# Optimization experiments

Hardware: AMD Instinct MI355X
Metric: run time of the kernel (lower is better)

Reference implementation:

```python
import math
import jax, jax.numpy as jnp
import numpy as np

N_NODES = 100000
N_EDGES = 1600000
IN_DIM, HID_DIM, OUT_DIM = 8, 64, 112


def _glorot(key, fan_in, fan_out):
    lim = math.sqrt(6.0 / (fan_in + fan_out))
    return jax.random.uniform(key, (fan_in, fan_out), jnp.float32, -lim, lim)


def _layer_params(key, in_d, out_d):
    ks = jax.random.split(key, 8)
    return dict(
        Wq=_glorot(ks[0], in_d, out_d), bq=jnp.zeros((out_d,), jnp.float32),
        Wk=_glorot(ks[1], in_d, out_d), bk=jnp.zeros((out_d,), jnp.float32),
        Wv=_glorot(ks[2], in_d, out_d), bv=jnp.zeros((out_d,), jnp.float32),
        Ws=_glorot(ks[3], in_d, out_d), bs=jnp.zeros((out_d,), jnp.float32),
    )


def setup_inputs() -> dict:
    key = jax.random.key(0)
    kx, ke, k0, k1, k2 = jax.random.split(key, 5)
    inp = {
        'x': jax.random.normal(kx, (N_NODES, IN_DIM), jnp.float32),
        'edge_index': jax.random.randint(ke, (2, N_EDGES), 0, N_NODES, jnp.int64),
    }
    for li, (kk, ind, outd) in enumerate([(k0, IN_DIM, HID_DIM), (k1, HID_DIM, HID_DIM), (k2, HID_DIM, OUT_DIM)]):
        p = _layer_params(kk, ind, outd)
        for name, v in p.items():
            inp[f'{name}{li}'] = v
    return inp


def _transformer_conv(x, src, dst, Wq, bq, Wk, bk, Wv, bv, Ws, bs):
    # heads=1, concat=True, no edge_attr, eval mode (no dropout)
    N = x.shape[0]
    C = Wq.shape[1]
    q = x @ Wq + bq            # [N, C]
    k = x @ Wk + bk
    v = x @ Wv + bv
    # per-edge attention score: <q_dst, k_src> / sqrt(C)
    scores = jnp.sum(q[dst] * k[src], axis=-1) * (1.0 / math.sqrt(C))  # [E]
    # segment softmax over destination neighborhoods (stable)
    m = jax.ops.segment_max(scores, dst, num_segments=N)               # [N]
    e = jnp.exp(scores - m[dst])                                       # [E]
    denom = jax.ops.segment_sum(e, dst, num_segments=N)                # [N]
    alpha = e / denom[dst]                                             # [E]
    # weighted scatter-add of source values to destinations
    out = jax.ops.segment_sum(alpha[:, None] * v[src], dst, num_segments=N)  # [N, C]
    # root/skip connection
    return out + (x @ Ws + bs)


def reference(x, edge_index,
              Wq0, bq0, Wk0, bk0, Wv0, bv0, Ws0, bs0,
              Wq1, bq1, Wk1, bk1, Wv1, bv1, Ws1, bs1,
              Wq2, bq2, Wk2, bk2, Wv2, bv2, Ws2, bs2):
    src, dst = edge_index[0], edge_index[1]
    h = _transformer_conv(x, src, dst, Wq0, bq0, Wk0, bk0, Wv0, bv0, Ws0, bs0)
    h = jax.nn.relu(h)
    h = _transformer_conv(h, src, dst, Wq1, bq1, Wk1, bk1, Wv1, bv1, Ws1, bs1)
    h = jax.nn.relu(h)
    out = _transformer_conv(h, src, dst, Wq2, bq2, Wk2, bk2, Wv2, bv2, Ws2, bs2)
    return out
```

## Files before the change

kernel.cpp:

```cpp
#include <hip/hip_runtime.h>
#include <hip/hip_fp16.h>
#include <math.h>
#include <float.h>
#include <stdint.h>

#define NN 100000
#define NE 1600000

#define SCAN_T 256
#define SCAN_E 1024
#define SCAN_NB ((NN + SCAN_E - 1) / SCAN_E)

#define NBUCK ((NN + 255) / 256)
#define EPB   4096
#define NBLK  ((NE + EPB - 1) / EPB)
#define HISTN (NBUCK * NBLK)
#define GS_NB ((HISTN + SCAN_E - 1) / SCAN_E)
#define BCAP  5120

typedef __attribute__((ext_vector_type(8))) short short8v;
typedef __attribute__((ext_vector_type(4))) float float4v;

__device__ __forceinline__ unsigned short f32_to_bf16_rne(float f) {
    unsigned u = __float_as_uint(f);
    u += 0x7FFFu + ((u >> 16) & 1u);
    return (unsigned short)(u >> 16);
}
__device__ __forceinline__ float bf16_to_f32(unsigned short h) {
    return __uint_as_float(((unsigned)h) << 16);
}

__device__ __forceinline__ void prep_one(int idx, int K, int OUT,
    const float* Wq, const float* Wk, const float* Wv, const float* Ws,
    unsigned short* wsp) {
    int NKS  = (K + 31) / 32;
    int j    = idx & 7;
    int lane = (idx >> 3) & 63;
    int cell = idx >> 9;
    int ks   = cell % NKS;
    int ct   = cell / NKS;
    int g = lane >> 4, ln = lane & 15;
    int k = ks * 32 + g * 8 + j;
    int c = ct * 16 + ln;
    int mat = c / OUT, cm = c % OUT;
    const float* W = (mat == 0) ? Wq : (mat == 1) ? Wk : (mat == 2) ? Wv : Ws;
    float f = (k < K) ? W[(size_t)k * OUT + cm] : 0.f;
    unsigned short h = f32_to_bf16_rne(f);
    float resid = f - bf16_to_f32(h);
    wsp[(size_t)cell * 1024 + lane * 8 + j]       = h;
    wsp[(size_t)cell * 1024 + 512 + lane * 8 + j] = f32_to_bf16_rne(resid);
}

#define PREP_N0 (16 * 1 * 512)
#define PREP_N1 (16 * 2 * 512)
#define PREP_N2 (28 * 2 * 512)
#define PREP_NT (PREP_N0 + PREP_N1 + PREP_N2)

__global__ __launch_bounds__(256)
void prep_w_all(const float* __restrict__ q0W, const float* __restrict__ k0W,
                const float* __restrict__ v0W, const float* __restrict__ s0W,
                const float* __restrict__ q1W, const float* __restrict__ k1W,
                const float* __restrict__ v1W, const float* __restrict__ s1W,
                const float* __restrict__ q2W, const float* __restrict__ k2W,
                const float* __restrict__ v2W, const float* __restrict__ s2W,
                unsigned short* __restrict__ wsp0,
                unsigned short* __restrict__ wsp1,
                unsigned short* __restrict__ wsp2) {
    int idx = blockIdx.x * 256 + threadIdx.x;
    if (idx < PREP_N0)
        prep_one(idx, 8, 64, q0W, k0W, v0W, s0W, wsp0);
    else if (idx < PREP_N0 + PREP_N1)
        prep_one(idx - PREP_N0, 64, 64, q1W, k1W, v1W, s1W, wsp1);
    else if (idx < PREP_NT)
        prep_one(idx - PREP_N0 - PREP_N1, 64, 112, q2W, k2W, v2W, s2W, wsp2);
}

template<int K, int OUT, int CTSPLIT>
__global__ __launch_bounds__(256)
void gemm_qkvs(const float* __restrict__ x,
               const unsigned short* __restrict__ wsp,
               const float* __restrict__ bq, const float* __restrict__ bk,
               const float* __restrict__ bv, const float* __restrict__ bs,
               float* __restrict__ q, unsigned short* __restrict__ kv,
               float* __restrict__ outskip) {
    constexpr int NKS  = (K + 31) / 32;
    constexpr int OUTT = 4 * OUT;
    constexpr int NCT  = OUTT / 16;
    constexpr int CTPB = NCT / CTSPLIT;

    const int t    = threadIdx.x;
    const int lane = t & 63;
    const int wv   = t >> 6;
    const int g    = lane >> 4;
    const int ln   = lane & 15;
    const int rowbase = (blockIdx.x * 4 + wv) * 32;
    if (rowbase >= NN) return;

    union F8 { short8v v; unsigned short s[8]; uint4 u4; };

    F8 ahi[2][NKS], alo[2][NKS];
#pragma unroll
    for (int rt = 0; rt < 2; ++rt) {
        int r = rowbase + rt * 16 + ln;
        if (r >= NN) r = NN - 1;
        const float* rowp = x + (size_t)r * K;
#pragma unroll
        for (int ks = 0; ks < NKS; ++ks) {
            const int k0 = ks * 32 + g * 8;
            float xv[8];
            if (k0 + 8 <= K) {
                float4 p0 = *(const float4*)(rowp + k0);
                float4 p1 = *(const float4*)(rowp + k0 + 4);
                xv[0] = p0.x; xv[1] = p0.y; xv[2] = p0.z; xv[3] = p0.w;
                xv[4] = p1.x; xv[5] = p1.y; xv[6] = p1.z; xv[7] = p1.w;
            } else {
#pragma unroll
                for (int j = 0; j < 8; ++j) xv[j] = 0.f;
            }
#pragma unroll
            for (int j = 0; j < 8; ++j) {
                unsigned short h = f32_to_bf16_rne(xv[j]);
                ahi[rt][ks].s[j] = h;
                alo[rt][ks].s[j] = f32_to_bf16_rne(xv[j] - bf16_to_f32(h));
            }
        }
    }

    const int ct0 = blockIdx.y * CTPB;
#pragma unroll 1
    for (int ct = ct0; ct < ct0 + CTPB; ++ct) {
        F8 bhi[NKS], blo[NKS];
        const unsigned short* wp = wsp + (size_t)(ct * NKS) * 1024 + lane * 8;
#pragma unroll
        for (int ks = 0; ks < NKS; ++ks) {
            bhi[ks].u4 = *(const uint4*)(wp + ks * 1024);
            blo[ks].u4 = *(const uint4*)(wp + ks * 1024 + 512);
        }

        const int cb  = ct * 16;
        const int mat = cb / OUT;
        const int cm  = (cb % OUT) + ln;
        const float* B = (mat == 0) ? bq : (mat == 1) ? bk : (mat == 2) ? bv : bs;
        const float bias = B[cm];
        float4v acc0 = {bias, bias, bias, bias};
        float4v acc1 = {bias, bias, bias, bias};
#pragma unroll
        for (int ks = 0; ks < NKS; ++ks) {
            acc0 = __builtin_amdgcn_mfma_f32_16x16x32_bf16(ahi[0][ks].v, blo[ks].v, acc0, 0, 0, 0);
            acc0 = __builtin_amdgcn_mfma_f32_16x16x32_bf16(alo[0][ks].v, bhi[ks].v, acc0, 0, 0, 0);
            acc0 = __builtin_amdgcn_mfma_f32_16x16x32_bf16(ahi[0][ks].v, bhi[ks].v, acc0, 0, 0, 0);
            acc1 = __builtin_amdgcn_mfma_f32_16x16x32_bf16(ahi[1][ks].v, blo[ks].v, acc1, 0, 0, 0);
            acc1 = __builtin_amdgcn_mfma_f32_16x16x32_bf16(alo[1][ks].v, bhi[ks].v, acc1, 0, 0, 0);
            acc1 = __builtin_amdgcn_mfma_f32_16x16x32_bf16(ahi[1][ks].v, bhi[ks].v, acc1, 0, 0, 0);
        }

        if (mat == 0 || mat == 3) {
            float* dst = (mat == 0) ? q : outskip;
#pragma unroll
            for (int rt = 0; rt < 2; ++rt) {
                float4v a = rt ? acc1 : acc0;
#pragma unroll
                for (int reg = 0; reg < 4; ++reg) {
                    int node = rowbase + rt * 16 + g * 4 + reg;
                    if (node < NN)
                        dst[(size_t)node * OUT + cm] = a[reg];
                }
            }
        } else {
            const int base = (mat == 1) ? 0 : 4;
            const int kvoff = ((cm >> 2) * 8) + (cm & 3) + base;
#pragma unroll
            for (int rt = 0; rt < 2; ++rt) {
                float4v a = rt ? acc1 : acc0;
#pragma unroll
                for (int reg = 0; reg < 4; ++reg) {
                    int node = rowbase + rt * 16 + g * 4 + reg;
                    float f = a[reg];
                    float other = __shfl_xor(f, 1);
                    if (node < NN && !(ln & 1)) {
                        unsigned lo16 = __half_as_ushort(__float2half_rn(f));
                        unsigned hi16 = __half_as_ushort(__float2half_rn(other));
                        *(unsigned*)(kv + (size_t)node * (2 * OUT) + kvoff)
                            = lo16 | (hi16 << 16);
                    }
                }
            }
        }
    }
}

__global__ __launch_bounds__(256)
void bin_count(const int* __restrict__ ei, int* __restrict__ hist) {
    __shared__ int h[NBUCK];
    const int t = threadIdx.x;
    for (int i = t; i < NBUCK; i += 256) h[i] = 0;
    __syncthreads();
    int e0 = blockIdx.x * EPB;
    int e1 = e0 + EPB < NE ? e0 + EPB : NE;
    for (int i = e0 + t; i < e1; i += 256)
        atomicAdd(&h[ei[NE + i] >> 8], 1);
    __syncthreads();
    for (int i = t; i < NBUCK; i += 256)
        hist[(size_t)i * NBLK + blockIdx.x] = h[i];
}

__global__ __launch_bounds__(SCAN_T)
void gscan1(int* __restrict__ a, int* __restrict__ bsums) {
    __shared__ int lds[SCAN_T];
    int t = threadIdx.x;
    int base = blockIdx.x * SCAN_E + t * 4;
    int vals[4];
    int s = 0;
#pragma unroll
    for (int j = 0; j < 4; ++j) {
        int idx = base + j;
        vals[j] = (idx < HISTN) ? a[idx] : 0;
        s += vals[j];
    }
    lds[t] = s;
    __syncthreads();
    for (int off = 1; off < SCAN_T; off <<= 1) {
        int xx = (t >= off) ? lds[t - off] : 0;
        __syncthreads();
        lds[t] += xx;
        __syncthreads();
    }
    int run = (t > 0) ? lds[t - 1] : 0;
    if (t == SCAN_T - 1) bsums[blockIdx.x] = lds[t];
#pragma unroll
    for (int j = 0; j < 4; ++j) {
        int idx = base + j;
        if (idx < HISTN) a[idx] = run;
        run += vals[j];
    }
}

__global__ __launch_bounds__(256)
void gscan2(int* __restrict__ bsums) {
    __shared__ int lds[256];
    int t = threadIdx.x;
    lds[t] = (t < GS_NB) ? bsums[t] : 0;
    __syncthreads();
    for (int off = 1; off < 256; off <<= 1) {
        int xx = (t >= off) ? lds[t - off] : 0;
        __syncthreads();
        lds[t] += xx;
        __syncthreads();
    }
    if (t < GS_NB) bsums[t] = (t > 0) ? lds[t - 1] : 0;
}

__global__ __launch_bounds__(256)
void gscan3(int* __restrict__ a, const int* __restrict__ bsums,
            int* __restrict__ bstart) {
    int i = blockIdx.x * 256 + threadIdx.x;
    if (i < HISTN) {
        int v = a[i] + bsums[i / SCAN_E];
        a[i] = v;
        if (i % NBLK == 0) bstart[i / NBLK] = v;
    }
    if (i == 0) bstart[NBUCK] = NE;
}

__global__ __launch_bounds__(256)
void bin_scatter(const int* __restrict__ ei, const int* __restrict__ hist,
                 unsigned* __restrict__ ebuf) {
    __shared__ int off[NBUCK];
    const int t = threadIdx.x;
    for (int i = t; i < NBUCK; i += 256)
        off[i] = hist[(size_t)i * NBLK + blockIdx.x];
    __syncthreads();
    int e0 = blockIdx.x * EPB;
    int e1 = e0 + EPB < NE ? e0 + EPB : NE;
    for (int i = e0 + t; i < e1; i += 256) {
        int src = ei[i];
        int dst = ei[NE + i];
        int b = dst >> 8;
        int p = atomicAdd(&off[b], 1);
        ebuf[p] = ((unsigned)(dst & 255) << 17) | (unsigned)src;
    }
}

__global__ __launch_bounds__(256)
void bucket_hist(const int* __restrict__ bstart,
                 const unsigned* __restrict__ ebuf,
                 int* __restrict__ counts) {
    __shared__ int h[256];
    const int b = blockIdx.x;
    const int t = threadIdx.x;
    h[t] = 0;
    __syncthreads();
    int beg = bstart[b], end = bstart[b + 1];
    for (int i = beg + t; i < end; i += 256)
        atomicAdd(&h[ebuf[i] >> 17], 1);
    __syncthreads();
    int d = b * 256 + t;
    if (d < NN) counts[d] = h[t];
}

__global__ __launch_bounds__(SCAN_T)
void scan1(const int* __restrict__ counts, int* __restrict__ offsets,
           int* __restrict__ blocksums) {
    __shared__ int lds[SCAN_T];
    int t = threadIdx.x;
    int base = blockIdx.x * SCAN_E + t * 4;
    int vals[4];
    int s = 0;
#pragma unroll
    for (int j = 0; j < 4; ++j) {
        int idx = base + j;
        vals[j] = (idx < NN) ? counts[idx] : 0;
        s += vals[j];
    }
    lds[t] = s;
    __syncthreads();
    for (int off = 1; off < SCAN_T; off <<= 1) {
        int xx = (t >= off) ? lds[t - off] : 0;
        __syncthreads();
        lds[t] += xx;
        __syncthreads();
    }
    int run = (t > 0) ? lds[t - 1] : 0;
    if (t == SCAN_T - 1) blocksums[blockIdx.x] = lds[t];
#pragma unroll
    for (int j = 0; j < 4; ++j) {
        int idx = base + j;
        if (idx < NN) offsets[idx] = run;
        run += vals[j];
    }
}

__global__ __launch_bounds__(128)
void scan2(int* __restrict__ blocksums) {
    __shared__ int lds[128];
    int t = threadIdx.x;
    lds[t] = (t < SCAN_NB) ? blocksums[t] : 0;
    __syncthreads();
    for (int off = 1; off < 128; off <<= 1) {
        int xx = (t >= off) ? lds[t - off] : 0;
        __syncthreads();
        lds[t] += xx;
        __syncthreads();
    }
    if (t < SCAN_NB) blocksums[t] = (t > 0) ? lds[t - 1] : 0;
}

__global__ __launch_bounds__(256)
void scan3(int* __restrict__ offsets, const int* __restrict__ blocksums) {
    int i = blockIdx.x * blockDim.x + threadIdx.x;
    if (i < NN) offsets[i] = offsets[i] + blocksums[i / SCAN_E];
    if (i == 0) offsets[NN] = NE;
}

__global__ __launch_bounds__(256)
void csr_write(const int* __restrict__ bstart,
               const unsigned* __restrict__ ebuf,
               const int* __restrict__ offsets,
               int* __restrict__ sorted_src) {
    __shared__ int h[256];
    __shared__ int pre[256];
    __shared__ int posi[256];
    __shared__ unsigned srt[BCAP];
    const int b = blockIdx.x;
    const int t = threadIdx.x;
    h[t] = 0;
    __syncthreads();
    int beg = bstart[b];
    int cnt = bstart[b + 1] - beg;
    cnt = cnt < BCAP ? cnt : BCAP;
    const unsigned* buf = ebuf + beg;
    for (int i = t; i < cnt; i += 256)
        atomicAdd(&h[buf[i] >> 17], 1);
    __syncthreads();
    int v = h[t];
    pre[t] = v;
    __syncthreads();
    for (int off = 1; off < 256; off <<= 1) {
        int xx = (t >= off) ? pre[t - off] : 0;
        __syncthreads();
        pre[t] += xx;
        __syncthreads();
    }
    posi[t] = pre[t] - v;
    __syncthreads();
    for (int i = t; i < cnt; i += 256) {
        unsigned u = buf[i];
        int dl = u >> 17;
        int p = atomicAdd(&posi[dl], 1);
        srt[p] = u & 0x1FFFFu;
    }
    __syncthreads();
    const int base = offsets[b << 8];
    for (int i = t; i < cnt; i += 256)
        sorted_src[base + i] = (int)srt[i];
}

__device__ __forceinline__ float row16_sum(float x) {
    int y;
    y = __builtin_amdgcn_update_dpp(0, __float_as_int(x), 0x121, 0xF, 0xF, true); x += __int_as_float(y);
    y = __builtin_amdgcn_update_dpp(0, __float_as_int(x), 0x122, 0xF, 0xF, true); x += __int_as_float(y);
    y = __builtin_amdgcn_update_dpp(0, __float_as_int(x), 0x124, 0xF, 0xF, true); x += __int_as_float(y);
    y = __builtin_amdgcn_update_dpp(0, __float_as_int(x), 0x128, 0xF, 0xF, true); x += __int_as_float(y);
    return x;
}

__device__ __forceinline__ float mix2(float acc, unsigned u, float q0, float q1) {
    __half2 h = *(__half2*)&u;
    acc = fmaf(__half2float(h.x), q0, acc);
    return fmaf(__half2float(h.y), q1, acc);
}
__device__ __forceinline__ void vmix2(float& a0, float& a1, unsigned u, float w) {
    __half2 h = *(__half2*)&u;
    a0 = fmaf(__half2float(h.x), w, a0);
    a1 = fmaf(__half2float(h.y), w, a1);
}

template<int C, bool RELU>
__global__ __launch_bounds__(128)
void attn_gather(const int* __restrict__ offsets,
                 const int* __restrict__ sorted_src,
                 const float* __restrict__ q,
                 const unsigned short* __restrict__ kv,
                 float* __restrict__ out, float scale) {
    const int wid  = (int)((blockIdx.x * blockDim.x + threadIdx.x) >> 6);
    const int lane = threadIdx.x & 63;
    if (wid >= NN) return;
    const int grp = lane >> 4;
    const int ch  = (lane & 15) * 4;
    constexpr bool P2 = (C > 64);
    const bool hi = P2 && (ch + 64 < C);

    const int beg = offsets[wid], end = offsets[wid + 1];

    const float sl = scale * 1.44269504f;
    float4 qv0 = *(const float4*)(q + (size_t)wid * C + ch);
    qv0.x *= sl; qv0.y *= sl; qv0.z *= sl; qv0.w *= sl;
    float4 qv1 = make_float4(0.f, 0.f, 0.f, 0.f);
    if (hi) {
        qv1 = *(const float4*)(q + (size_t)wid * C + ch + 64);
        qv1.x *= sl; qv1.y *= sl; qv1.z *= sl; qv1.w *= sl;
    }

    float m = -FLT_MAX, l = 0.f;
    float4 a0 = make_float4(0.f, 0.f, 0.f, 0.f);
    float4 a1 = make_float4(0.f, 0.f, 0.f, 0.f);

    const unsigned short* kvch = kv + 2 * ch;
    const uint4 zz = make_uint4(0, 0, 0, 0);

    int i = beg + grp;
    while (i < end) {
        uint4 t0[4], t1[4];
#pragma unroll
        for (int j = 0; j < 4; ++j) {
            t0[j] = zz; t1[j] = zz;
            int idx = i + 4 * j;
            if (idx < end) {
                const unsigned short* row = kvch + (size_t)sorted_src[idx] * (2 * C);
                t0[j] = *(const uint4*)(row);
                if (hi) t1[j] = *(const uint4*)(row + 128);
            }
        }
        float s[4];
#pragma unroll
        for (int j = 0; j < 4; ++j) {
            float part = 0.f;
            part = mix2(part, t0[j].x, qv0.x, qv0.y);
            part = mix2(part, t0[j].y, qv0.z, qv0.w);
            if (P2) {
                part = mix2(part, t1[j].x, qv1.x, qv1.y);
                part = mix2(part, t1[j].y, qv1.z, qv1.w);
            }
            part = row16_sum(part);
            s[j] = (i + 4 * j < end) ? part : -FLT_MAX;
        }
        float mn = fmaxf(m, fmaxf(fmaxf(s[0], s[1]), fmaxf(s[2], s[3])));
        float al = __builtin_amdgcn_exp2f(m - mn);
        float w[4];
#pragma unroll
        for (int j = 0; j < 4; ++j)
            w[j] = __builtin_amdgcn_exp2f(s[j] - mn);
        l = l * al + ((w[0] + w[1]) + (w[2] + w[3]));
        a0.x *= al; a0.y *= al; a0.z *= al; a0.w *= al;
        if (P2) { a1.x *= al; a1.y *= al; a1.z *= al; a1.w *= al; }
#pragma unroll
        for (int j = 0; j < 4; ++j) {
            vmix2(a0.x, a0.y, t0[j].z, w[j]);
            vmix2(a0.z, a0.w, t0[j].w, w[j]);
            if (P2) {
                vmix2(a1.x, a1.y, t1[j].z, w[j]);
                vmix2(a1.z, a1.w, t1[j].w, w[j]);
            }
        }
        m = mn;
        i += 16;
    }

#pragma unroll
    for (int d = 16; d <= 32; d <<= 1) {
        float mo = __shfl_xor(m, d);
        float lo = __shfl_xor(l, d);
        float4 ao0, ao1;
        ao0.x = __shfl_xor(a0.x, d); ao0.y = __shfl_xor(a0.y, d);
        ao0.z = __shfl_xor(a0.z, d); ao0.w = __shfl_xor(a0.w, d);
        if (P2) {
            ao1.x = __shfl_xor(a1.x, d); ao1.y = __shfl_xor(a1.y, d);
            ao1.z = __shfl_xor(a1.z, d); ao1.w = __shfl_xor(a1.w, d);
        }
        float mn = fmaxf(m, mo);
        float e1 = (l  > 0.f) ? __builtin_amdgcn_exp2f(m  - mn) : 0.f;
        float e2 = (lo > 0.f) ? __builtin_amdgcn_exp2f(mo - mn) : 0.f;
        l = l * e1 + lo * e2;
        a0.x = a0.x * e1 + ao0.x * e2; a0.y = a0.y * e1 + ao0.y * e2;
        a0.z = a0.z * e1 + ao0.z * e2; a0.w = a0.w * e1 + ao0.w * e2;
        if (P2) {
            a1.x = a1.x * e1 + ao1.x * e2; a1.y = a1.y * e1 + ao1.y * e2;
            a1.z = a1.z * e1 + ao1.z * e2; a1.w = a1.w * e1 + ao1.w * e2;
        }
        m = mn;
    }

    if (lane < 16) {
        float inv = (l > 0.f) ? 1.f / l : 0.f;
        size_t o = (size_t)wid * C + ch;
        float4 sk = *(const float4*)(out + o);
        float4 r;
        r.x = sk.x + a0.x * inv; r.y = sk.y + a0.y * inv;
        r.z = sk.z + a0.z * inv; r.w = sk.w + a0.w * inv;
        if (RELU) {
            r.x = fmaxf(r.x, 0.f); r.y = fmaxf(r.y, 0.f);
            r.z = fmaxf(r.z, 0.f); r.w = fmaxf(r.w, 0.f);
        }
        *(float4*)(out + o) = r;
        if (hi) {
            float4 sk1 = *(const float4*)(out + o + 64);
            float4 r1;
            r1.x = sk1.x + a1.x * inv; r1.y = sk1.y + a1.y * inv;
            r1.z = sk1.z + a1.z * inv; r1.w = sk1.w + a1.w * inv;
            if (RELU) {
                r1.x = fmaxf(r1.x, 0.f); r1.y = fmaxf(r1.y, 0.f);
                r1.z = fmaxf(r1.z, 0.f); r1.w = fmaxf(r1.w, 0.f);
            }
            *(float4*)(out + o + 64) = r1;
        }
    }
}

template<int K, int OUT, bool RELU>
static void run_layer(const float* xin, const unsigned short* wsp,
                      const float* const* Wb,
                      const int* offsets, const int* sorted_src,
                      float* q, unsigned short* kv,
                      float* out, hipStream_t stream) {
    constexpr int CTSPLIT = 2;
    dim3 gg((NN + 127) / 128, CTSPLIT);
    gemm_qkvs<K, OUT, CTSPLIT><<<gg, 256, 0, stream>>>(
        xin, wsp, Wb[1], Wb[3], Wb[5], Wb[7], q, kv, out);

    float scale = 1.0f / sqrtf((float)OUT);
    attn_gather<OUT, RELU><<<(NN + 1) / 2, 128, 0, stream>>>(
        offsets, sorted_src, q, kv, out, scale);
}

extern "C" void kernel_launch(void* const* d_in, const int* in_sizes, int n_in,
                              void* d_out, int out_size, void* d_ws, size_t ws_size,
                              hipStream_t stream) {
    const float* x  = (const float*)d_in[0];
    const int*   ei = (const int*)d_in[1];
    const float* Wb0[8], *Wb1[8], *Wb2[8];
    for (int i = 0; i < 8; ++i) {
        Wb0[i] = (const float*)d_in[2 + i];
        Wb1[i] = (const float*)d_in[10 + i];
        Wb2[i] = (const float*)d_in[18 + i];
    }
    float* out = (float*)d_out;

    char* ws = (char*)d_ws;
    const size_t CMAX = 112;
    size_t off = 0;
    float*          q  = (float*)(ws + off);          off += (size_t)NN * CMAX * 4;
    unsigned short* kv = (unsigned short*)(ws + off); off += (size_t)NN * 2 * CMAX * 2;
    float* h0          = (float*)(ws + off);          off += (size_t)NN * 64 * 4;
    float* h1          = (float*)(ws + off);          off += (size_t)NN * 64 * 4;
    int*   sorted_src  = (int*)(ws + off);            off += (size_t)NE * 4;
    int*   counts      = (int*)(ws + off);            off += (size_t)NN * 4;
    int*   offsets     = (int*)(ws + off);            off += (size_t)(NN + 1) * 4;
    int*   blocksums   = (int*)(ws + off);            off += (size_t)SCAN_NB * 4;
    int*   hist        = (int*)(ws + off);            off += (size_t)HISTN * 4;
    int*   gsums       = (int*)(ws + off);            off += (size_t)GS_NB * 4;
    int*   bstart      = (int*)(ws + off);            off += (size_t)(NBUCK + 1) * 4;
    unsigned* ebuf     = (unsigned*)(ws + off);       off += (size_t)NE * 4;
    (void)ws_size; (void)in_sizes; (void)n_in; (void)out_size;

    bin_count<<<NBLK, 256, 0, stream>>>(ei, hist);
    gscan1<<<GS_NB, SCAN_T, 0, stream>>>(hist, gsums);
    gscan2<<<1, 256, 0, stream>>>(gsums);
    gscan3<<<(HISTN + 255) / 256, 256, 0, stream>>>(hist, gsums, bstart);
    bin_scatter<<<NBLK, 256, 0, stream>>>(ei, hist, ebuf);
    bucket_hist<<<NBUCK, 256, 0, stream>>>(bstart, ebuf, counts);
    scan1<<<SCAN_NB, SCAN_T, 0, stream>>>(counts, offsets, blocksums);
    scan2<<<1, 128, 0, stream>>>(blocksums);
    scan3<<<(NN + 255) / 256, 256, 0, stream>>>(offsets, blocksums);
    csr_write<<<NBUCK, 256, 0, stream>>>(bstart, ebuf, offsets, sorted_src);

    unsigned short* wspbase =
        (unsigned short*)(((uintptr_t)ebuf + 255) & ~(uintptr_t)255);
    unsigned short* wsp0 = wspbase;
    unsigned short* wsp1 = wsp0 + 16 * 1 * 1024;
    unsigned short* wsp2 = wsp1 + 16 * 2 * 1024;
    prep_w_all<<<(PREP_NT + 255) / 256, 256, 0, stream>>>(
        Wb0[0], Wb0[2], Wb0[4], Wb0[6],
        Wb1[0], Wb1[2], Wb1[4], Wb1[6],
        Wb2[0], Wb2[2], Wb2[4], Wb2[6],
        wsp0, wsp1, wsp2);

    run_layer<8,  64, true >(x,  wsp0, Wb0, offsets, sorted_src, q, kv, h0,  stream);
    run_layer<64, 64, true >(h0, wsp1, Wb1, offsets, sorted_src, q, kv, h1,  stream);
    run_layer<64, 112, false>(h1, wsp2, Wb2, offsets, sorted_src, q, kv, out, stream);
}
```

Measured before the change: 540.9 us.

## Fold per-node offset computation into csr_write and drop GEMM column split

csr_write already builds a per-bucket histogram and local prefix, so it now writes the global CSR offsets directly as bucket start plus local exclusive prefix. This removes the bucket_hist pass and the three-kernel scan over node counts, along with their extra reads of ebuf and four launches. Separately, the QKVS GEMM no longer splits column tiles across a second grid dimension: each block loops over all column tiles. That halves the grid but makes each block reuse its converted A fragments across twice as many tiles, trading parallelism for fewer redundant loads and bf16 conversions of x.

New measurement: 524.4 us. 3.0% less time.

```diff
diff --git a/kernel.cpp b/kernel.cpp
--- a/kernel.cpp
+++ b/kernel.cpp
@@ -9,7 +9,6 @@
 
 #define SCAN_T 256
 #define SCAN_E 1024
-#define SCAN_NB ((NN + SCAN_E - 1) / SCAN_E)
 
 #define NBUCK ((NN + 255) / 256)
 #define EPB   4096
@@ -75,7 +74,7 @@
         prep_one(idx - PREP_N0 - PREP_N1, 64, 112, q2W, k2W, v2W, s2W, wsp2);
 }
 
-template<int K, int OUT, int CTSPLIT>
+template<int K, int OUT>
 __global__ __launch_bounds__(256)
 void gemm_qkvs(const float* __restrict__ x,
                const unsigned short* __restrict__ wsp,
@@ -86,7 +85,6 @@
     constexpr int NKS  = (K + 31) / 32;
     constexpr int OUTT = 4 * OUT;
     constexpr int NCT  = OUTT / 16;
-    constexpr int CTPB = NCT / CTSPLIT;
 
     const int t    = threadIdx.x;
     const int lane = t & 63;
@@ -126,9 +124,8 @@
         }
     }
 
-    const int ct0 = blockIdx.y * CTPB;
 #pragma unroll 1
-    for (int ct = ct0; ct < ct0 + CTPB; ++ct) {
+    for (int ct = 0; ct < NCT; ++ct) {
         F8 bhi[NKS], blo[NKS];
         const unsigned short* wp = wsp + (size_t)(ct * NKS) * 1024 + lane * 8;
 #pragma unroll
@@ -282,80 +279,9 @@
 }
 
 __global__ __launch_bounds__(256)
-void bucket_hist(const int* __restrict__ bstart,
-                 const unsigned* __restrict__ ebuf,
-                 int* __restrict__ counts) {
-    __shared__ int h[256];
-    const int b = blockIdx.x;
-    const int t = threadIdx.x;
-    h[t] = 0;
-    __syncthreads();
-    int beg = bstart[b], end = bstart[b + 1];
-    for (int i = beg + t; i < end; i += 256)
-        atomicAdd(&h[ebuf[i] >> 17], 1);
-    __syncthreads();
-    int d = b * 256 + t;
-    if (d < NN) counts[d] = h[t];
-}
-
-__global__ __launch_bounds__(SCAN_T)
-void scan1(const int* __restrict__ counts, int* __restrict__ offsets,
-           int* __restrict__ blocksums) {
-    __shared__ int lds[SCAN_T];
-    int t = threadIdx.x;
-    int base = blockIdx.x * SCAN_E + t * 4;
-    int vals[4];
-    int s = 0;
-#pragma unroll
-    for (int j = 0; j < 4; ++j) {
-        int idx = base + j;
-        vals[j] = (idx < NN) ? counts[idx] : 0;
-        s += vals[j];
-    }
-    lds[t] = s;
-    __syncthreads();
-    for (int off = 1; off < SCAN_T; off <<= 1) {
-        int xx = (t >= off) ? lds[t - off] : 0;
-        __syncthreads();
-        lds[t] += xx;
-        __syncthreads();
-    }
-    int run = (t > 0) ? lds[t - 1] : 0;
-    if (t == SCAN_T - 1) blocksums[blockIdx.x] = lds[t];
-#pragma unroll
-    for (int j = 0; j < 4; ++j) {
-        int idx = base + j;
-        if (idx < NN) offsets[idx] = run;
-        run += vals[j];
-    }
-}
-
-__global__ __launch_bounds__(128)
-void scan2(int* __restrict__ blocksums) {
-    __shared__ int lds[128];
-    int t = threadIdx.x;
-    lds[t] = (t < SCAN_NB) ? blocksums[t] : 0;
-    __syncthreads();
-    for (int off = 1; off < 128; off <<= 1) {
-        int xx = (t >= off) ? lds[t - off] : 0;
-        __syncthreads();
-        lds[t] += xx;
-        __syncthreads();
-    }
-    if (t < SCAN_NB) blocksums[t] = (t > 0) ? lds[t - 1] : 0;
-}
-
-__global__ __launch_bounds__(256)
-void scan3(int* __restrict__ offsets, const int* __restrict__ blocksums) {
-    int i = blockIdx.x * blockDim.x + threadIdx.x;
-    if (i < NN) offsets[i] = offsets[i] + blocksums[i / SCAN_E];
-    if (i == 0) offsets[NN] = NE;
-}
-
-__global__ __launch_bounds__(256)
 void csr_write(const int* __restrict__ bstart,
                const unsigned* __restrict__ ebuf,
-               const int* __restrict__ offsets,
+               int* __restrict__ offsets,
                int* __restrict__ sorted_src) {
     __shared__ int h[256];
     __shared__ int pre[256];
@@ -381,7 +307,11 @@
         pre[t] += xx;
         __syncthreads();
     }
-    posi[t] = pre[t] - v;
+    int excl = pre[t] - v;
+    posi[t] = excl;
+    int d = b * 256 + t;
+    if (d < NN) offsets[d] = beg + excl;
+    if (b == NBUCK - 1 && t == 0) offsets[NN] = NE;
     __syncthreads();
     for (int i = t; i < cnt; i += 256) {
         unsigned u = buf[i];
@@ -390,9 +320,8 @@
         srt[p] = u & 0x1FFFFu;
     }
     __syncthreads();
-    const int base = offsets[b << 8];
     for (int i = t; i < cnt; i += 256)
-        sorted_src[base + i] = (int)srt[i];
+        sorted_src[beg + i] = (int)srt[i];
 }
 
 __device__ __forceinline__ float row16_sum(float x) {
@@ -552,9 +481,7 @@
                       const int* offsets, const int* sorted_src,
                       float* q, unsigned short* kv,
                       float* out, hipStream_t stream) {
-    constexpr int CTSPLIT = 2;
-    dim3 gg((NN + 127) / 128, CTSPLIT);
-    gemm_qkvs<K, OUT, CTSPLIT><<<gg, 256, 0, stream>>>(
+    gemm_qkvs<K, OUT><<<(NN + 127) / 128, 256, 0, stream>>>(
         xin, wsp, Wb[1], Wb[3], Wb[5], Wb[7], q, kv, out);
 
     float scale = 1.0f / sqrtf((float)OUT);
@@ -583,9 +510,7 @@
     float* h0          = (float*)(ws + off);          off += (size_t)NN * 64 * 4;
     float* h1          = (float*)(ws + off);          off += (size_t)NN * 64 * 4;
     int*   sorted_src  = (int*)(ws + off);            off += (size_t)NE * 4;
-    int*   counts      = (int*)(ws + off);            off += (size_t)NN * 4;
     int*   offsets     = (int*)(ws + off);            off += (size_t)(NN + 1) * 4;
-    int*   blocksums   = (int*)(ws + off);            off += (size_t)SCAN_NB * 4;
     int*   hist        = (int*)(ws + off);            off += (size_t)HISTN * 4;
     int*   gsums       = (int*)(ws + off);            off += (size_t)GS_NB * 4;
     int*   bstart      = (int*)(ws + off);            off += (size_t)(NBUCK + 1) * 4;
@@ -597,10 +522,6 @@
     gscan2<<<1, 256, 0, stream>>>(gsums);
     gscan3<<<(HISTN + 255) / 256, 256, 0, stream>>>(hist, gsums, bstart);
     bin_scatter<<<NBLK, 256, 0, stream>>>(ei, hist, ebuf);
-    bucket_hist<<<NBUCK, 256, 0, stream>>>(bstart, ebuf, counts);
-    scan1<<<SCAN_NB, SCAN_T, 0, stream>>>(counts, offsets, blocksums);
-    scan2<<<1, 128, 0, stream>>>(blocksums);
-    scan3<<<(NN + 255) / 256, 256, 0, stream>>>(offsets, blocksums);
     csr_write<<<NBUCK, 256, 0, stream>>>(bstart, ebuf, offsets, sorted_src);
 
     unsigned short* wspbase =
```
